# Optimization experiments

Measured on AMD Instinct MI355X. Metric: run time of the kernel, lower is better.

The kernel has to match this reference:

```python
import jax, jax.numpy as jnp
import numpy as np

B, S, D, H, DH = 4, 2048, 1024, 16, 64
INIT_STD = 0.02
IGNORE = -100000.0


def setup_inputs() -> dict:
    key = jax.random.key(0)
    ks = jax.random.split(key, 5)
    x = jax.random.normal(ks[0], (B, S, D), dtype=jnp.float32)
    W_Q = INIT_STD * jax.random.normal(ks[1], (H, D, DH), dtype=jnp.float32)
    W_K = INIT_STD * jax.random.normal(ks[2], (H, D, DH), dtype=jnp.float32)
    W_V = INIT_STD * jax.random.normal(ks[3], (H, D, DH), dtype=jnp.float32)
    W_O = INIT_STD * jax.random.normal(ks[4], (H, DH, D), dtype=jnp.float32)
    b_Q = jnp.zeros((H, DH), dtype=jnp.float32)
    b_K = jnp.zeros((H, DH), dtype=jnp.float32)
    b_V = jnp.zeros((H, DH), dtype=jnp.float32)
    b_O = jnp.zeros((D,), dtype=jnp.float32)
    return {"x": x, "W_Q": W_Q, "b_Q": b_Q, "W_K": W_K, "b_K": b_K,
            "W_V": W_V, "b_V": b_V, "W_O": W_O, "b_O": b_O}


def reference(x, W_Q, b_Q, W_K, b_K, W_V, b_V, W_O, b_O):
    # x: (B, S, D); projections -> (B, S, H, DH)
    Q = jnp.einsum('bqd,hde->bqhe', x, W_Q) + b_Q
    K = jnp.einsum('bkd,hde->bkhe', x, W_K) + b_K
    V = jnp.einsum('bkd,hde->bkhe', x, W_V) + b_V
    d_head = Q.shape[-1]
    # scores: (B, H, Sq, Sk)
    scores = jnp.einsum('bqhe,bkhe->bhqk', Q, K) / np.sqrt(d_head).astype(np.float32)
    s = scores.shape[-1]
    causal = jnp.triu(jnp.ones((s, s), dtype=bool), k=1)
    scores = jnp.where(causal, jnp.float32(IGNORE), scores)
    A = jax.nn.softmax(scores, axis=-1)
    z = jnp.einsum('bhqk,bkhe->bqhe', A, V)
    # output projection: sum over heads + bias
    attn_out = jnp.einsum('bqhe,hed->bqd', z, W_O) + b_O
    return attn_out
```

## Files before the change

kernel.cpp:

```cpp
#include <hip/hip_runtime.h>


#define B_ 4
#define S_ 2048
#define D_ 1024
#define H_ 16
#define DH_ 64

typedef unsigned short ushort_t;
typedef __attribute__((ext_vector_type(4))) short short4v;
typedef __attribute__((ext_vector_type(8))) short short8v;
typedef __attribute__((ext_vector_type(4))) float floatx4;
typedef __attribute__((ext_vector_type(4))) unsigned short ushort4v;

static __device__ __forceinline__ ushort_t f2bf(float f) {
    union { float f; unsigned u; } v; v.f = f;
    unsigned r = v.u + 0x7fffu + ((v.u >> 16) & 1u);
    return (ushort_t)(r >> 16);
}

static __device__ __forceinline__ float fast_exp2(float x) {
#if __has_builtin(__builtin_amdgcn_exp2f)
    return __builtin_amdgcn_exp2f(x);
#else
    return exp2f(x);
#endif
}

static __device__ __forceinline__ unsigned pack_bf16_tr(float lo, float hi) {
    union { float f; unsigned u; } a, b;
    a.f = lo; b.f = hi;
    return __builtin_amdgcn_perm(b.u, a.u, 0x07060302u);
}

static __device__ __forceinline__ void g2lds16(const void* g, void* l) {
    __builtin_amdgcn_global_load_lds(
        (__attribute__((address_space(1))) void*)(unsigned long long)(size_t)g,
        (__attribute__((address_space(3))) void*)(unsigned int)(size_t)l,
        16, 0, 0);
}

__global__ void prep_kernel(const float* __restrict__ x,
                            const float* __restrict__ wq, const float* __restrict__ wk,
                            const float* __restrict__ wv, const float* __restrict__ wo,
                            ushort_t* __restrict__ xb, ushort_t* __restrict__ wt,
                            ushort_t* __restrict__ wot) {
    __shared__ float tile[32][33];
    int bid = blockIdx.x;
    int tid = threadIdx.x;
    if (bid < 8192) {
        int i = (bid * 256 + tid) * 4;
        float4 v = *(const float4*)&x[i];
        ushort4v o;
        o[0] = f2bf(v.x); o[1] = f2bf(v.y); o[2] = f2bf(v.z); o[3] = f2bf(v.w);
        *(ushort4v*)&xb[i] = o;
        return;
    }
    const float* src;
    ushort_t* d;
    int C, r0, c0;
    if (bid < 11264) {
        int t = bid - 8192;
        int z = t / 64, r = t % 64;
        src = (z < 16 ? wq : (z < 32 ? wk : wv)) + (size_t)(z & 15) * 65536;
        d = wt + (size_t)z * 65536;
        C = 64; r0 = (r >> 1) * 32; c0 = (r & 1) * 32;
    } else {
        int t = bid - 11264;
        int z = t / 64, r = t % 64;
        src = wo + (size_t)z * 65536;
        d = wot + (size_t)z * 64;
        C = 1024; r0 = (r & 1) * 32; c0 = (r >> 1) * 32;
    }
    int tx = tid & 31, ty = tid >> 5;
#pragma unroll
    for (int i = 0; i < 4; ++i)
        tile[ty + i * 8][tx] = src[(size_t)(r0 + ty + i * 8) * C + c0 + tx];
    __syncthreads();
#pragma unroll
    for (int i = 0; i < 4; ++i)
        d[(size_t)(c0 + ty + i * 8) * 1024 + r0 + tx] = f2bf(tile[tx][ty + i * 8]);
}


#define GQ_BAR() __builtin_amdgcn_s_barrier()
#define GQ_VM4 do { asm volatile("s_waitcnt vmcnt(4)"); __builtin_amdgcn_sched_barrier(0); } while (0)
#define GQ_VM1 do { asm volatile("s_waitcnt vmcnt(1)"); __builtin_amdgcn_sched_barrier(0); } while (0)
#define GQ_VM0 do { asm volatile("s_waitcnt vmcnt(0)"); __builtin_amdgcn_sched_barrier(0); } while (0)
#define GQ_WAITLG do { asm volatile("s_waitcnt lgkmcnt(0)"); __builtin_amdgcn_sched_barrier(0); } while (0)

#define GQ_READS_B(KB)                                                          \
    _Pragma("unroll") for (int nt = 0; nt < 4; ++nt)                            \
        bfr[KB][nt] = *(const short8v*)&cB[(wn * 64 + nt * 16) * 64 + ((KB) ? kb1 : kb0)];

#define GQ_READS_A(MH, KB)                                                      \
    _Pragma("unroll") for (int i = 0; i < 2; ++i)                               \
        af[i] = *(const short8v*)&cA[(wm * 64 + ((MH) * 2 + i) * 16) * 64 + ((KB) ? kb1 : kb0)];

#define GQ_MFMA(MH, KB)                                                         \
    GQ_WAITLG;                                                                  \
    __builtin_amdgcn_s_setprio(1);                                              \
    _Pragma("unroll") for (int i = 0; i < 2; ++i)                               \
        _Pragma("unroll") for (int nt = 0; nt < 4; ++nt)                        \
            acc[(MH) * 2 + i][nt] = __builtin_amdgcn_mfma_f32_16x16x32_bf16(    \
                af[i], bfr[KB][nt], acc[(MH) * 2 + i][nt], 0, 0, 0);            \
    __builtin_amdgcn_s_setprio(0);                                              \
    __builtin_amdgcn_sched_barrier(0);

#define GQ_KSTEP(CA, CB, S1, S2, S3, S4, WMID, WEND) do {                       \
    const ushort_t* cA = (CA); const ushort_t* cB = (CB);                       \
    short8v af[2]; short8v bfr[2][4];                                           \
    GQ_READS_B(0) GQ_READS_A(0, 0) S1; GQ_BAR();                                \
    GQ_MFMA(0, 0) GQ_BAR();                                                     \
    GQ_READS_B(1) GQ_READS_A(0, 1) S2; GQ_BAR();                                \
    GQ_MFMA(0, 1) WMID; GQ_BAR();                                               \
    GQ_READS_A(1, 0) S3; GQ_BAR();                                              \
    GQ_MFMA(1, 0) GQ_BAR();                                                     \
    GQ_READS_A(1, 1) S4; GQ_BAR();                                              \
    GQ_MFMA(1, 1) WEND; GQ_BAR();                                               \
} while (0)

__global__ __launch_bounds__(512, 2) void gemm_qkv(const ushort_t* __restrict__ A,
                                                   const ushort_t* __restrict__ Wt,
                                                   const float* __restrict__ bq,
                                                   const float* __restrict__ bk,
                                                   const float* __restrict__ bv,
                                                   ushort_t* __restrict__ Qw,
                                                   ushort_t* __restrict__ Kw,
                                                   ushort_t* __restrict__ Vw) {
    __shared__ ushort_t sA[2][128 * 64];
    __shared__ ushort_t sB[2][256 * 64];
    const int tid = threadIdx.x;
    const int lane = tid & 63, w = tid >> 6;
    const int lq = lane & 15, quad = lane >> 4;
    const int wm = w >> 2, wn = w & 3;
    const int m0 = blockIdx.x * 128, n0 = blockIdx.y * 256;

    const int kb0 = lq * 64 + ((quad ^ (lq & 7)) << 3);
    const int kb1 = lq * 64 + (((4 | quad) ^ (lq & 7)) << 3);

    const int uRA = ((w >> 2) << 6) + (w & 3) * 8;

    auto stageA1 = [&](ushort_t* dst, int kk, int R0) __attribute__((always_inline)) {
        int rr = R0 + (lane >> 3);
        int cc = (lane & 7) ^ (rr & 7);
        g2lds16(&A[(size_t)(m0 + rr) * 1024 + kk + cc * 8], &dst[R0 * 64]);
    };
    auto stageB1 = [&](ushort_t* dst, int kk, int R0) __attribute__((always_inline)) {
        int rr = R0 + (lane >> 3);
        int cc = (lane & 7) ^ (rr & 7);
        g2lds16(&Wt[(size_t)(n0 + rr) * 1024 + kk + cc * 8], &dst[R0 * 64]);
    };

    floatx4 acc[4][4] = {};

    stageA1(sA[0], 0, uRA);
    stageB1(sB[0], 0, w * 32);
    stageB1(sB[0], 0, w * 32 + 8);
    stageB1(sB[0], 0, w * 32 + 16);
    stageB1(sB[0], 0, w * 32 + 24);
    stageA1(sA[0], 0, uRA + 32);
    GQ_VM1;
    GQ_BAR();

    int p = 0;
    for (int t = 0; t < 15; ++t) {
        const int kk = (t + 1) * 64;
        ushort_t* nA = sA[p ^ 1];
        ushort_t* nB = sB[p ^ 1];
        GQ_KSTEP(sA[p], sB[p],
                 { stageA1(nA, kk, uRA); stageB1(nB, kk, w * 32); },
                 { stageB1(nB, kk, w * 32 + 8); stageB1(nB, kk, w * 32 + 16); },
                 { stageB1(nB, kk, w * 32 + 24); },
                 { stageA1(nA, kk, uRA + 32); },
                 GQ_VM4, GQ_VM1);
        p ^= 1;
    }
    GQ_KSTEP(sA[1], sB[1], (void)0, (void)0, (void)0, (void)0, GQ_VM0, (void)0);

    const int mat = blockIdx.y >> 2;
    const float* bias = mat == 0 ? bq : (mat == 1 ? bk : bv);
    const int colbase = (blockIdx.y & 3) * 256 + wn * 64;
    float bias_v[4];
#pragma unroll
    for (int nt = 0; nt < 4; ++nt) bias_v[nt] = bias[colbase + nt * 16 + lq];

#pragma unroll
    for (int mt = 0; mt < 4; ++mt) {
#pragma unroll
        for (int nt = 0; nt < 4; ++nt) {
            int row0 = m0 + wm * 64 + mt * 16 + quad * 4;
            int col = colbase + nt * 16 + lq;
            int h = col >> 6, e = col & 63;
            if (mat == 2) {
                int b = row0 >> 11, s = row0 & 2047;
                ushort4v pk;
#pragma unroll
                for (int rg = 0; rg < 4; ++rg) pk[rg] = f2bf(acc[mt][nt][rg] + bias_v[nt]);
                *(ushort4v*)&Vw[((size_t)((b << 4) | h) * 64 + e) * 2048 + s] = pk;
            } else {
                ushort_t* Du = mat == 0 ? Qw : Kw;
#pragma unroll
                for (int rg = 0; rg < 4; ++rg) {
                    int row = row0 + rg;
                    int b = row >> 11, s = row & 2047;
                    float v = acc[mt][nt][rg] + bias_v[nt];
                    if (mat == 0) v *= 0.18033688011112042f;
                    Du[((size_t)((b << 4) | h) * 2048 + s) * 64 + e] = f2bf(v);
                }
            }
        }
    }
}

#define VROW 140
__global__ __launch_bounds__(256) void attn_kernel(const ushort_t* __restrict__ Q,
                                                   const ushort_t* __restrict__ Kg,
                                                   const ushort_t* __restrict__ Vt,
                                                   ushort_t* __restrict__ Z) {
    __shared__ ushort_t sK[2][128 * 64];
    __shared__ ushort_t sV[64 * VROW];
    const int tid = threadIdx.x;
    const int lane = tid & 63, w = tid >> 6;
    const int lq = lane & 15, quad = lane >> 4;
    const int bh = blockIdx.x;
    const int b = bh >> 4, h = bh & 15;
    const ushort_t* Qp = Q + (size_t)bh * S_ * DH_;
    const ushort_t* Kp = Kg + (size_t)bh * S_ * DH_;
    const ushort_t* Vp = Vt + (size_t)bh * DH_ * S_;

    const int kbase0 = lq * 64 + ((quad ^ (lq & 7)) << 3);
    const int kbase1 = lq * 64 + (((4 | quad) ^ (lq & 7)) << 3);
    const int vbase = lq * VROW + quad * 4;
    const int vr = w * 16 + (lane >> 2);
    const int vc = (lane & 3) * 32;

    const floatx4 fzero = {0.f, 0.f, 0.f, 0.f};

    auto stageK = [&](int kt, int bs) __attribute__((always_inline)) {
        ushort_t* dK = sK[bs];
#pragma unroll
        for (int p = 0; p < 4; ++p) {
            int rrk = w * 32 + p * 8 + (lane >> 3);
            int ck = (lane & 7) ^ (rrk & 7);
            g2lds16(&Kp[(size_t)(kt * 128 + rrk) * 64 + ck * 8], &dK[(w * 32 + p * 8) * 64]);
        }
    };
    auto loadV = [&](int kt, short8v* vr4) __attribute__((always_inline)) {
        const ushort_t* src = &Vp[(size_t)vr * 2048 + kt * 128 + vc];
#pragma unroll
        for (int j = 0; j < 4; ++j) vr4[j] = *(const short8v*)&src[j * 8];
    };
    auto writeV = [&](const short8v* vr4) __attribute__((always_inline)) {
        ushort_t* dst = &sV[vr * VROW + vc];
#pragma unroll
        for (int j = 0; j < 4; ++j) *(short8v*)&dst[j * 8] = vr4[j];
    };

    for (int pass = 0; pass < 2; ++pass) {
        const int qt = pass == 0 ? (int)blockIdx.y : 15 - (int)blockIdx.y;
        const int q0 = qt * 128;

        short8v qf[2][2];
#pragma unroll
        for (int qi = 0; qi < 2; ++qi)
#pragma unroll
            for (int ks = 0; ks < 2; ++ks)
                qf[qi][ks] = *(const short8v*)&Qp[(size_t)(q0 + w * 32 + qi * 16 + lq) * DH_ + ks * 32 + quad * 8];

        float l_i[2] = {0.f, 0.f};
        floatx4 o[2][4] = {};
        short8v vreg[4];

        stageK(0, 0);
        loadV(0, vreg);

        for (int kt = 0; kt <= qt; ++kt) {
            const bool diag = (kt == qt);
            const ushort_t* cK = sK[kt & 1];

            __syncthreads();
            writeV(vreg);
            if (kt < qt) {
                stageK(kt + 1, (kt + 1) & 1);
                loadV(kt + 1, vreg);
            }

            floatx4 st[8][2];
            __builtin_amdgcn_s_setprio(1);
#pragma unroll
            for (int si = 0; si < 8; ++si) {
                short8v a0 = *(const short8v*)&cK[kbase0 + si * 1024];
                short8v a1 = *(const short8v*)&cK[kbase1 + si * 1024];
#pragma unroll
                for (int qi = 0; qi < 2; ++qi) {
                    st[si][qi] = __builtin_amdgcn_mfma_f32_16x16x32_bf16(a0, qf[qi][0], fzero, 0, 0, 0);
                    st[si][qi] = __builtin_amdgcn_mfma_f32_16x16x32_bf16(a1, qf[qi][1], st[si][qi], 0, 0, 0);
                }
            }
            __builtin_amdgcn_s_setprio(0);

            short4v pf[8][2];
#pragma unroll
            for (int qi = 0; qi < 2; ++qi) {
                const int qg = q0 + w * 32 + qi * 16 + lq;
                float lsum = 0.f;
#pragma unroll
                for (int si = 0; si < 8; ++si) {
                    float p[4];
#pragma unroll
                    for (int rg = 0; rg < 4; ++rg) {
                        float v = st[si][qi][rg];
                        if (diag) {
                            int sg = kt * 128 + si * 16 + quad * 4 + rg;
                            if (sg > qg) v = -1e30f;
                        }
                        p[rg] = fast_exp2(v);
                        lsum += p[rg];
                    }
                    union { unsigned u[2]; short4v v4; } pk;
                    pk.u[0] = pack_bf16_tr(p[0], p[1]);
                    pk.u[1] = pack_bf16_tr(p[2], p[3]);
                    pf[si][qi] = pk.v4;
                }
                l_i[qi] += lsum;
            }

            __syncthreads();

            __builtin_amdgcn_s_setprio(1);
#pragma unroll
            for (int ksp = 0; ksp < 8; ++ksp) {
#pragma unroll
                for (int et = 0; et < 4; ++et) {
                    short4v vf = *(const short4v*)&sV[vbase + et * (16 * VROW) + ksp * 16];
#pragma unroll
                    for (int qi = 0; qi < 2; ++qi)
                        o[qi][et] = __builtin_amdgcn_mfma_f32_16x16x16bf16_1k(pf[ksp][qi], vf, o[qi][et], 0, 0, 0);
                }
            }
            __builtin_amdgcn_s_setprio(0);
        }

#pragma unroll
        for (int qi = 0; qi < 2; ++qi) {
            float lf = l_i[qi];
            lf += __shfl_xor(lf, 16);
            lf += __shfl_xor(lf, 32);
            float linv[4];
#pragma unroll
            for (int rg = 0; rg < 4; ++rg) linv[rg] = 1.0f / __shfl(lf, quad * 4 + rg);
#pragma unroll
            for (int et = 0; et < 4; ++et) {
#pragma unroll
                for (int rg = 0; rg < 4; ++rg) {
                    int qg = q0 + w * 32 + qi * 16 + quad * 4 + rg;
                    int e = et * 16 + lq;
                    Z[((size_t)(b * S_ + qg) * H_ + h) * DH_ + e] = f2bf(o[qi][et][rg] * linv[rg]);
                }
            }
        }
    }
}

__global__ __launch_bounds__(256) void gemm_o(const ushort_t* __restrict__ A,
                                              const ushort_t* __restrict__ Bt,
                                              const float* __restrict__ bias,
                                              float* __restrict__ Dst) {
    __shared__ ushort_t sA[128 * 64];
    __shared__ ushort_t sB[128 * 64];
    const int tid = threadIdx.x;
    const int lane = tid & 63, w = tid >> 6;
    const int lq = lane & 15, quad = lane >> 4;
    const int wm = w >> 1, wn = w & 1;
    const int m0 = blockIdx.x * 128, n0 = blockIdx.y * 128;

    floatx4 acc[4][4] = {};

    for (int k0 = 0; k0 < 1024; k0 += 64) {
        __syncthreads();
#pragma unroll
        for (int p = 0; p < 4; ++p) {
            int rr = w * 32 + p * 8 + (lane >> 3);
            int cc = (lane & 7) ^ (rr & 7);
            g2lds16(&A[(size_t)(m0 + rr) * 1024 + k0 + cc * 8], &sA[(w * 32 + p * 8) * 64]);
            g2lds16(&Bt[(size_t)(n0 + rr) * 1024 + k0 + cc * 8], &sB[(w * 32 + p * 8) * 64]);
        }
        __syncthreads();
#pragma unroll
        for (int ks = 0; ks < 2; ++ks) {
            short8v af[4], bfr[4];
#pragma unroll
            for (int t = 0; t < 4; ++t) {
                int ma = wm * 64 + t * 16 + lq;
                af[t] = *(const short8v*)&sA[ma * 64 + ((((ks << 2) | quad) ^ (ma & 7)) << 3)];
                int nb = wn * 64 + t * 16 + lq;
                bfr[t] = *(const short8v*)&sB[nb * 64 + ((((ks << 2) | quad) ^ (nb & 7)) << 3)];
            }
#pragma unroll
            for (int mt = 0; mt < 4; ++mt)
#pragma unroll
                for (int nt = 0; nt < 4; ++nt)
                    acc[mt][nt] = __builtin_amdgcn_mfma_f32_16x16x32_bf16(af[mt], bfr[nt], acc[mt][nt], 0, 0, 0);
        }
    }

    float bias_v[4];
#pragma unroll
    for (int nt = 0; nt < 4; ++nt) bias_v[nt] = bias[n0 + wn * 64 + nt * 16 + lq];

#pragma unroll
    for (int mt = 0; mt < 4; ++mt) {
#pragma unroll
        for (int nt = 0; nt < 4; ++nt) {
            int row0 = m0 + wm * 64 + mt * 16 + quad * 4;
            int col = n0 + wn * 64 + nt * 16 + lq;
#pragma unroll
            for (int rg = 0; rg < 4; ++rg)
                Dst[(size_t)(row0 + rg) * 1024 + col] = acc[mt][nt][rg] + bias_v[nt];
        }
    }
}

extern "C" void kernel_launch(void* const* d_in, const int* in_sizes, int n_in,
                              void* d_out, int out_size, void* d_ws, size_t ws_size,
                              hipStream_t stream) {
    const float* x  = (const float*)d_in[0];
    const float* wq = (const float*)d_in[1];
    const float* bq = (const float*)d_in[2];
    const float* wk = (const float*)d_in[3];
    const float* bk = (const float*)d_in[4];
    const float* wv = (const float*)d_in[5];
    const float* bv = (const float*)d_in[6];
    const float* wo = (const float*)d_in[7];
    const float* bo = (const float*)d_in[8];

    char* ws = (char*)d_ws;
    size_t off = 0;
    ushort_t* xb  = (ushort_t*)(ws + off); off += (size_t)8192 * 1024 * 2;
    ushort_t* wt  = (ushort_t*)(ws + off); off += (size_t)3 * 1024 * 1024 * 2;
    ushort_t* wot = (ushort_t*)(ws + off); off += (size_t)1024 * 1024 * 2;
    ushort_t* Qw  = (ushort_t*)(ws + off); off += (size_t)8192 * 1024 * 2;
    ushort_t* Kw  = (ushort_t*)(ws + off); off += (size_t)8192 * 1024 * 2;
    ushort_t* Vw  = (ushort_t*)(ws + off); off += (size_t)8192 * 1024 * 2;
    ushort_t* Zw  = (ushort_t*)(ws + off); off += (size_t)8192 * 1024 * 2;

    prep_kernel<<<12288, 256, 0, stream>>>(x, wq, wk, wv, wo, xb, wt, wot);
    gemm_qkv<<<dim3(64, 12), 512, 0, stream>>>(xb, wt, bq, bk, bv, Qw, Kw, Vw);
    attn_kernel<<<dim3(64, 8), 256, 0, stream>>>(Qw, Kw, Vw, Zw);
    gemm_o<<<dim3(64, 8), 256, 0, stream>>>(Zw, wot, bo, (float*)d_out);
}
```

Baseline: 262.6 us.

## Reuse pipelined QKV GEMM body for output projection; split attention pairs into single tiles

The output-projection GEMM now uses the same double-buffered 128x256 tile with 512 threads and an interleaved MFMA/load schedule as the QKV GEMM, factored into a shared macro. The attention kernel no longer pairs a light and a heavy causal query tile per block. It launches one block per query tile, heaviest first, with a launch-bounds occupancy hint of 3 and no s_setprio calls. This aims to hide load latency in the O GEMM and improve attention occupancy and scheduling, at the cost of some load imbalance and fewer O-GEMM blocks.

```diff
diff --git a/kernel.cpp b/kernel.cpp
--- a/kernel.cpp
+++ b/kernel.cpp
@@ -120,6 +120,30 @@
     GQ_MFMA(1, 1) WEND; GQ_BAR();                                               \
 } while (0)
 
+#define GQ_BODY(APTR, BPTR)                                                     \
+    stageA1(sA[0], 0, uRA);                                                     \
+    stageB1(sB[0], 0, w * 32);                                                  \
+    stageB1(sB[0], 0, w * 32 + 8);                                              \
+    stageB1(sB[0], 0, w * 32 + 16);                                             \
+    stageB1(sB[0], 0, w * 32 + 24);                                             \
+    stageA1(sA[0], 0, uRA + 32);                                                \
+    GQ_VM1;                                                                     \
+    GQ_BAR();                                                                   \
+    int p = 0;                                                                  \
+    for (int t = 0; t < 15; ++t) {                                              \
+        const int kk = (t + 1) * 64;                                            \
+        ushort_t* nA = sA[p ^ 1];                                               \
+        ushort_t* nB = sB[p ^ 1];                                               \
+        GQ_KSTEP(sA[p], sB[p],                                                  \
+                 { stageA1(nA, kk, uRA); stageB1(nB, kk, w * 32); },            \
+                 { stageB1(nB, kk, w * 32 + 8); stageB1(nB, kk, w * 32 + 16); },\
+                 { stageB1(nB, kk, w * 32 + 24); },                             \
+                 { stageA1(nA, kk, uRA + 32); },                                \
+                 GQ_VM4, GQ_VM1);                                               \
+        p ^= 1;                                                                 \
+    }                                                                           \
+    GQ_KSTEP(sA[1], sB[1], (void)0, (void)0, (void)0, (void)0, GQ_VM0, (void)0);
+
 __global__ __launch_bounds__(512, 2) void gemm_qkv(const ushort_t* __restrict__ A,
                                                    const ushort_t* __restrict__ Wt,
                                                    const float* __restrict__ bq,
@@ -154,29 +178,7 @@
 
     floatx4 acc[4][4] = {};
 
-    stageA1(sA[0], 0, uRA);
-    stageB1(sB[0], 0, w * 32);
-    stageB1(sB[0], 0, w * 32 + 8);
-    stageB1(sB[0], 0, w * 32 + 16);
-    stageB1(sB[0], 0, w * 32 + 24);
-    stageA1(sA[0], 0, uRA + 32);
-    GQ_VM1;
-    GQ_BAR();
-
-    int p = 0;
-    for (int t = 0; t < 15; ++t) {
-        const int kk = (t + 1) * 64;
-        ushort_t* nA = sA[p ^ 1];
-        ushort_t* nB = sB[p ^ 1];
-        GQ_KSTEP(sA[p], sB[p],
-                 { stageA1(nA, kk, uRA); stageB1(nB, kk, w * 32); },
-                 { stageB1(nB, kk, w * 32 + 8); stageB1(nB, kk, w * 32 + 16); },
-                 { stageB1(nB, kk, w * 32 + 24); },
-                 { stageA1(nA, kk, uRA + 32); },
-                 GQ_VM4, GQ_VM1);
-        p ^= 1;
-    }
-    GQ_KSTEP(sA[1], sB[1], (void)0, (void)0, (void)0, (void)0, GQ_VM0, (void)0);
+    GQ_BODY(A, Wt)
 
     const int mat = blockIdx.y >> 2;
     const float* bias = mat == 0 ? bq : (mat == 1 ? bk : bv);
@@ -214,10 +216,10 @@
 }
 
 #define VROW 140
-__global__ __launch_bounds__(256) void attn_kernel(const ushort_t* __restrict__ Q,
-                                                   const ushort_t* __restrict__ Kg,
-                                                   const ushort_t* __restrict__ Vt,
-                                                   ushort_t* __restrict__ Z) {
+__global__ __launch_bounds__(256, 3) void attn_kernel(const ushort_t* __restrict__ Q,
+                                                      const ushort_t* __restrict__ Kg,
+                                                      const ushort_t* __restrict__ Vt,
+                                                      ushort_t* __restrict__ Z) {
     __shared__ ushort_t sK[2][128 * 64];
     __shared__ ushort_t sV[64 * VROW];
     const int tid = threadIdx.x;
@@ -257,164 +259,148 @@
         for (int j = 0; j < 4; ++j) *(short8v*)&dst[j * 8] = vr4[j];
     };
 
-    for (int pass = 0; pass < 2; ++pass) {
-        const int qt = pass == 0 ? (int)blockIdx.y : 15 - (int)blockIdx.y;
-        const int q0 = qt * 128;
-
-        short8v qf[2][2];
-#pragma unroll
-        for (int qi = 0; qi < 2; ++qi)
-#pragma unroll
-            for (int ks = 0; ks < 2; ++ks)
-                qf[qi][ks] = *(const short8v*)&Qp[(size_t)(q0 + w * 32 + qi * 16 + lq) * DH_ + ks * 32 + quad * 8];
-
-        float l_i[2] = {0.f, 0.f};
-        floatx4 o[2][4] = {};
-        short8v vreg[4];
-
-        stageK(0, 0);
-        loadV(0, vreg);
-
-        for (int kt = 0; kt <= qt; ++kt) {
-            const bool diag = (kt == qt);
-            const ushort_t* cK = sK[kt & 1];
-
-            __syncthreads();
-            writeV(vreg);
-            if (kt < qt) {
-                stageK(kt + 1, (kt + 1) & 1);
-                loadV(kt + 1, vreg);
+    const int qt = 15 - (int)blockIdx.y;
+    const int q0 = qt * 128;
+
+    short8v qf[2][2];
+#pragma unroll
+    for (int qi = 0; qi < 2; ++qi)
+#pragma unroll
+        for (int ks = 0; ks < 2; ++ks)
+            qf[qi][ks] = *(const short8v*)&Qp[(size_t)(q0 + w * 32 + qi * 16 + lq) * DH_ + ks * 32 + quad * 8];
+
+    float l_i[2] = {0.f, 0.f};
+    floatx4 o[2][4] = {};
+    short8v vreg[4];
+
+    stageK(0, 0);
+    loadV(0, vreg);
+
+    for (int kt = 0; kt <= qt; ++kt) {
+        const bool diag = (kt == qt);
+        const ushort_t* cK = sK[kt & 1];
+
+        __syncthreads();
+        writeV(vreg);
+        if (kt < qt) {
+            stageK(kt + 1, (kt + 1) & 1);
+            loadV(kt + 1, vreg);
+        }
+
+        floatx4 st[8][2];
+#pragma unroll
+        for (int si = 0; si < 8; ++si) {
+            short8v a0 = *(const short8v*)&cK[kbase0 + si * 1024];
+            short8v a1 = *(const short8v*)&cK[kbase1 + si * 1024];
+#pragma unroll
+            for (int qi = 0; qi < 2; ++qi) {
+                st[si][qi] = __builtin_amdgcn_mfma_f32_16x16x32_bf16(a0, qf[qi][0], fzero, 0, 0, 0);
+                st[si][qi] = __builtin_amdgcn_mfma_f32_16x16x32_bf16(a1, qf[qi][1], st[si][qi], 0, 0, 0);
             }
-
-            floatx4 st[8][2];
-            __builtin_amdgcn_s_setprio(1);
+        }
+
+        short4v pf[8][2];
+#pragma unroll
+        for (int qi = 0; qi < 2; ++qi) {
+            const int qg = q0 + w * 32 + qi * 16 + lq;
+            float lsum = 0.f;
 #pragma unroll
             for (int si = 0; si < 8; ++si) {
-                short8v a0 = *(const short8v*)&cK[kbase0 + si * 1024];
-                short8v a1 = *(const short8v*)&cK[kbase1 + si * 1024];
-#pragma unroll
-                for (int qi = 0; qi < 2; ++qi) {
-                    st[si][qi] = __builtin_amdgcn_mfma_f32_16x16x32_bf16(a0, qf[qi][0], fzero, 0, 0, 0);
-                    st[si][qi] = __builtin_amdgcn_mfma_f32_16x16x32_bf16(a1, qf[qi][1], st[si][qi], 0, 0, 0);
+                float p[4];
+#pragma unroll
+                for (int rg = 0; rg < 4; ++rg) {
+                    float v = st[si][qi][rg];
+                    if (diag) {
+                        int sg = kt * 128 + si * 16 + quad * 4 + rg;
+                        if (sg > qg) v = -1e30f;
+                    }
+                    p[rg] = fast_exp2(v);
+                    lsum += p[rg];
                 }
+                union { unsigned u[2]; short4v v4; } pk;
+                pk.u[0] = pack_bf16_tr(p[0], p[1]);
+                pk.u[1] = pack_bf16_tr(p[2], p[3]);
+                pf[si][qi] = pk.v4;
             }
-            __builtin_amdgcn_s_setprio(0);
-
-            short4v pf[8][2];
-#pragma unroll
-            for (int qi = 0; qi < 2; ++qi) {
-                const int qg = q0 + w * 32 + qi * 16 + lq;
-                float lsum = 0.f;
-#pragma unroll
-                for (int si = 0; si < 8; ++si) {
-                    float p[4];
-#pragma unroll
-                    for (int rg = 0; rg < 4; ++rg) {
-                        float v = st[si][qi][rg];
-                        if (diag) {
-                            int sg = kt * 128 + si * 16 + quad * 4 + rg;
-                            if (sg > qg) v = -1e30f;
-                        }
-                        p[rg] = fast_exp2(v);
-                        lsum += p[rg];
-                    }
-                    union { unsigned u[2]; short4v v4; } pk;
-                    pk.u[0] = pack_bf16_tr(p[0], p[1]);
-                    pk.u[1] = pack_bf16_tr(p[2], p[3]);
-                    pf[si][qi] = pk.v4;
-                }
-                l_i[qi] += lsum;
+            l_i[qi] += lsum;
+        }
+
+        __syncthreads();
+
+#pragma unroll
+        for (int ksp = 0; ksp < 8; ++ksp) {
+#pragma unroll
+            for (int et = 0; et < 4; ++et) {
+                short4v vf = *(const short4v*)&sV[vbase + et * (16 * VROW) + ksp * 16];
+#pragma unroll
+                for (int qi = 0; qi < 2; ++qi)
+                    o[qi][et] = __builtin_amdgcn_mfma_f32_16x16x16bf16_1k(pf[ksp][qi], vf, o[qi][et], 0, 0, 0);
             }
-
-            __syncthreads();
-
-            __builtin_amdgcn_s_setprio(1);
-#pragma unroll
-            for (int ksp = 0; ksp < 8; ++ksp) {
-#pragma unroll
-                for (int et = 0; et < 4; ++et) {
-                    short4v vf = *(const short4v*)&sV[vbase + et * (16 * VROW) + ksp * 16];
-#pragma unroll
-                    for (int qi = 0; qi < 2; ++qi)
-                        o[qi][et] = __builtin_amdgcn_mfma_f32_16x16x16bf16_1k(pf[ksp][qi], vf, o[qi][et], 0, 0, 0);
-                }
+        }
+    }
+
+#pragma unroll
+    for (int qi = 0; qi < 2; ++qi) {
+        float lf = l_i[qi];
+        lf += __shfl_xor(lf, 16);
+        lf += __shfl_xor(lf, 32);
+        float linv[4];
+#pragma unroll
+        for (int rg = 0; rg < 4; ++rg) linv[rg] = 1.0f / __shfl(lf, quad * 4 + rg);
+#pragma unroll
+        for (int et = 0; et < 4; ++et) {
+#pragma unroll
+            for (int rg = 0; rg < 4; ++rg) {
+                int qg = q0 + w * 32 + qi * 16 + quad * 4 + rg;
+                int e = et * 16 + lq;
+                Z[((size_t)(b * S_ + qg) * H_ + h) * DH_ + e] = f2bf(o[qi][et][rg] * linv[rg]);
             }
-            __builtin_amdgcn_s_setprio(0);
-        }
-
-#pragma unroll
-        for (int qi = 0; qi < 2; ++qi) {
-            float lf = l_i[qi];
-            lf += __shfl_xor(lf, 16);
-            lf += __shfl_xor(lf, 32);
-            float linv[4];
-#pragma unroll
-            for (int rg = 0; rg < 4; ++rg) linv[rg] = 1.0f / __shfl(lf, quad * 4 + rg);
-#pragma unroll
-            for (int et = 0; et < 4; ++et) {
-#pragma unroll
-                for (int rg = 0; rg < 4; ++rg) {
-                    int qg = q0 + w * 32 + qi * 16 + quad * 4 + rg;
-                    int e = et * 16 + lq;
-                    Z[((size_t)(b * S_ + qg) * H_ + h) * DH_ + e] = f2bf(o[qi][et][rg] * linv[rg]);
-                }
-            }
-        }
-    }
-}
-
-__global__ __launch_bounds__(256) void gemm_o(const ushort_t* __restrict__ A,
-                                              const ushort_t* __restrict__ Bt,
-                                              const float* __restrict__ bias,
-                                              float* __restrict__ Dst) {
-    __shared__ ushort_t sA[128 * 64];
-    __shared__ ushort_t sB[128 * 64];
+        }
+    }
+}
+
+__global__ __launch_bounds__(512, 2) void gemm_o(const ushort_t* __restrict__ A,
+                                                 const ushort_t* __restrict__ Bt,
+                                                 const float* __restrict__ bias,
+                                                 float* __restrict__ Dst) {
+    __shared__ ushort_t sA[2][128 * 64];
+    __shared__ ushort_t sB[2][256 * 64];
     const int tid = threadIdx.x;
     const int lane = tid & 63, w = tid >> 6;
     const int lq = lane & 15, quad = lane >> 4;
-    const int wm = w >> 1, wn = w & 1;
-    const int m0 = blockIdx.x * 128, n0 = blockIdx.y * 128;
+    const int wm = w >> 2, wn = w & 3;
+    const int m0 = blockIdx.x * 128, n0 = blockIdx.y * 256;
+
+    const int kb0 = lq * 64 + ((quad ^ (lq & 7)) << 3);
+    const int kb1 = lq * 64 + (((4 | quad) ^ (lq & 7)) << 3);
+    const int uRA = ((w >> 2) << 6) + (w & 3) * 8;
+
+    auto stageA1 = [&](ushort_t* dst, int kk, int R0) __attribute__((always_inline)) {
+        int rr = R0 + (lane >> 3);
+        int cc = (lane & 7) ^ (rr & 7);
+        g2lds16(&A[(size_t)(m0 + rr) * 1024 + kk + cc * 8], &dst[R0 * 64]);
+    };
+    auto stageB1 = [&](ushort_t* dst, int kk, int R0) __attribute__((always_inline)) {
+        int rr = R0 + (lane >> 3);
+        int cc = (lane & 7) ^ (rr & 7);
+        g2lds16(&Bt[(size_t)(n0 + rr) * 1024 + kk + cc * 8], &dst[R0 * 64]);
+    };
 
     floatx4 acc[4][4] = {};
 
-    for (int k0 = 0; k0 < 1024; k0 += 64) {
-        __syncthreads();
-#pragma unroll
-        for (int p = 0; p < 4; ++p) {
-            int rr = w * 32 + p * 8 + (lane >> 3);
-            int cc = (lane & 7) ^ (rr & 7);
-            g2lds16(&A[(size_t)(m0 + rr) * 1024 + k0 + cc * 8], &sA[(w * 32 + p * 8) * 64]);
-            g2lds16(&Bt[(size_t)(n0 + rr) * 1024 + k0 + cc * 8], &sB[(w * 32 + p * 8) * 64]);
-        }
-        __syncthreads();
-#pragma unroll
-        for (int ks = 0; ks < 2; ++ks) {
-            short8v af[4], bfr[4];
-#pragma unroll
-            for (int t = 0; t < 4; ++t) {
-                int ma = wm * 64 + t * 16 + lq;
-                af[t] = *(const short8v*)&sA[ma * 64 + ((((ks << 2) | quad) ^ (ma & 7)) << 3)];
-                int nb = wn * 64 + t * 16 + lq;
-                bfr[t] = *(const short8v*)&sB[nb * 64 + ((((ks << 2) | quad) ^ (nb & 7)) << 3)];
-            }
-#pragma unroll
-            for (int mt = 0; mt < 4; ++mt)
-#pragma unroll
-                for (int nt = 0; nt < 4; ++nt)
-                    acc[mt][nt] = __builtin_amdgcn_mfma_f32_16x16x32_bf16(af[mt], bfr[nt], acc[mt][nt], 0, 0, 0);
-        }
-    }
-
+    GQ_BODY(A, Bt)
+
+    const int colbase = n0 + wn * 64;
     float bias_v[4];
 #pragma unroll
-    for (int nt = 0; nt < 4; ++nt) bias_v[nt] = bias[n0 + wn * 64 + nt * 16 + lq];
+    for (int nt = 0; nt < 4; ++nt) bias_v[nt] = bias[colbase + nt * 16 + lq];
 
 #pragma unroll
     for (int mt = 0; mt < 4; ++mt) {
 #pragma unroll
         for (int nt = 0; nt < 4; ++nt) {
             int row0 = m0 + wm * 64 + mt * 16 + quad * 4;
-            int col = n0 + wn * 64 + nt * 16 + lq;
+            int col = colbase + nt * 16 + lq;
 #pragma unroll
             for (int rg = 0; rg < 4; ++rg)
                 Dst[(size_t)(row0 + rg) * 1024 + col] = acc[mt][nt][rg] + bias_v[nt];
@@ -447,6 +433,6 @@
 
     prep_kernel<<<12288, 256, 0, stream>>>(x, wq, wk, wv, wo, xb, wt, wot);
     gemm_qkv<<<dim3(64, 12), 512, 0, stream>>>(xb, wt, bq, bk, bv, Qw, Kw, Vw);
-    attn_kernel<<<dim3(64, 8), 256, 0, stream>>>(Qw, Kw, Vw, Zw);
-    gemm_o<<<dim3(64, 8), 256, 0, stream>>>(Zw, wot, bo, (float*)d_out);
-}
+    attn_kernel<<<dim3(64, 16), 256, 0, stream>>>(Qw, Kw, Vw, Zw);
+    gemm_o<<<dim3(64, 4), 512, 0, stream>>>(Zw, wot, bo, (float*)d_out);
+}
```

After: 295.8 us. 1.13x slower.

## Shrink QKV GEMM tile to 128x128 with 4 waves and drop attention setprio

Applied to the files above, without the earlier changes.

The QKV projection GEMM moves from 512-thread blocks with 128x256 tiles to 256-thread blocks with 128x128 tiles. The grid doubles in the N dimension, and the staging loads and vmcnt waits are rebalanced to match. This gives more, smaller blocks and less LDS per block, which should improve occupancy and wave scheduling, at the cost of reloading the A tile more often. Separately, the s_setprio raises around the MFMA sections in the attention kernel are removed.

```diff
diff --git a/kernel.cpp b/kernel.cpp
--- a/kernel.cpp
+++ b/kernel.cpp
@@ -85,7 +85,7 @@
 
 #define GQ_BAR() __builtin_amdgcn_s_barrier()
 #define GQ_VM4 do { asm volatile("s_waitcnt vmcnt(4)"); __builtin_amdgcn_sched_barrier(0); } while (0)
-#define GQ_VM1 do { asm volatile("s_waitcnt vmcnt(1)"); __builtin_amdgcn_sched_barrier(0); } while (0)
+#define GQ_VM2 do { asm volatile("s_waitcnt vmcnt(2)"); __builtin_amdgcn_sched_barrier(0); } while (0)
 #define GQ_VM0 do { asm volatile("s_waitcnt vmcnt(0)"); __builtin_amdgcn_sched_barrier(0); } while (0)
 #define GQ_WAITLG do { asm volatile("s_waitcnt lgkmcnt(0)"); __builtin_amdgcn_sched_barrier(0); } while (0)
 
@@ -120,7 +120,7 @@
     GQ_MFMA(1, 1) WEND; GQ_BAR();                                               \
 } while (0)
 
-__global__ __launch_bounds__(512, 2) void gemm_qkv(const ushort_t* __restrict__ A,
+__global__ __launch_bounds__(256, 2) void gemm_qkv(const ushort_t* __restrict__ A,
                                                    const ushort_t* __restrict__ Wt,
                                                    const float* __restrict__ bq,
                                                    const float* __restrict__ bk,
@@ -129,24 +129,25 @@
                                                    ushort_t* __restrict__ Kw,
                                                    ushort_t* __restrict__ Vw) {
     __shared__ ushort_t sA[2][128 * 64];
-    __shared__ ushort_t sB[2][256 * 64];
+    __shared__ ushort_t sB[2][128 * 64];
     const int tid = threadIdx.x;
     const int lane = tid & 63, w = tid >> 6;
     const int lq = lane & 15, quad = lane >> 4;
-    const int wm = w >> 2, wn = w & 3;
-    const int m0 = blockIdx.x * 128, n0 = blockIdx.y * 256;
+    const int wm = w >> 1, wn = w & 1;
+    const int m0 = blockIdx.x * 128, n0 = blockIdx.y * 128;
 
     const int kb0 = lq * 64 + ((quad ^ (lq & 7)) << 3);
     const int kb1 = lq * 64 + (((4 | quad) ^ (lq & 7)) << 3);
 
-    const int uRA = ((w >> 2) << 6) + (w & 3) * 8;
-
-    auto stageA1 = [&](ushort_t* dst, int kk, int R0) __attribute__((always_inline)) {
+    const int uA = ((w >> 1) << 6) + ((w & 1) << 4);
+    const int bR = w * 32;
+
+    auto stA = [&](ushort_t* dst, int kk, int R0) __attribute__((always_inline)) {
         int rr = R0 + (lane >> 3);
         int cc = (lane & 7) ^ (rr & 7);
         g2lds16(&A[(size_t)(m0 + rr) * 1024 + kk + cc * 8], &dst[R0 * 64]);
     };
-    auto stageB1 = [&](ushort_t* dst, int kk, int R0) __attribute__((always_inline)) {
+    auto stB = [&](ushort_t* dst, int kk, int R0) __attribute__((always_inline)) {
         int rr = R0 + (lane >> 3);
         int cc = (lane & 7) ^ (rr & 7);
         g2lds16(&Wt[(size_t)(n0 + rr) * 1024 + kk + cc * 8], &dst[R0 * 64]);
@@ -154,13 +155,11 @@
 
     floatx4 acc[4][4] = {};
 
-    stageA1(sA[0], 0, uRA);
-    stageB1(sB[0], 0, w * 32);
-    stageB1(sB[0], 0, w * 32 + 8);
-    stageB1(sB[0], 0, w * 32 + 16);
-    stageB1(sB[0], 0, w * 32 + 24);
-    stageA1(sA[0], 0, uRA + 32);
-    GQ_VM1;
+    stA(sA[0], 0, uA); stA(sA[0], 0, uA + 8);
+    stB(sB[0], 0, bR); stB(sB[0], 0, bR + 8);
+    stB(sB[0], 0, bR + 16); stB(sB[0], 0, bR + 24);
+    stA(sA[0], 0, uA + 32); stA(sA[0], 0, uA + 40);
+    GQ_VM2;
     GQ_BAR();
 
     int p = 0;
@@ -169,18 +168,18 @@
         ushort_t* nA = sA[p ^ 1];
         ushort_t* nB = sB[p ^ 1];
         GQ_KSTEP(sA[p], sB[p],
-                 { stageA1(nA, kk, uRA); stageB1(nB, kk, w * 32); },
-                 { stageB1(nB, kk, w * 32 + 8); stageB1(nB, kk, w * 32 + 16); },
-                 { stageB1(nB, kk, w * 32 + 24); },
-                 { stageA1(nA, kk, uRA + 32); },
-                 GQ_VM4, GQ_VM1);
+                 { stA(nA, kk, uA); stA(nA, kk, uA + 8); },
+                 { stB(nB, kk, bR); stB(nB, kk, bR + 8); },
+                 { stB(nB, kk, bR + 16); stB(nB, kk, bR + 24); },
+                 { stA(nA, kk, uA + 32); stA(nA, kk, uA + 40); },
+                 GQ_VM4, GQ_VM2);
         p ^= 1;
     }
     GQ_KSTEP(sA[1], sB[1], (void)0, (void)0, (void)0, (void)0, GQ_VM0, (void)0);
 
-    const int mat = blockIdx.y >> 2;
+    const int mat = blockIdx.y >> 3;
     const float* bias = mat == 0 ? bq : (mat == 1 ? bk : bv);
-    const int colbase = (blockIdx.y & 3) * 256 + wn * 64;
+    const int colbase = (blockIdx.y & 7) * 128 + wn * 64;
     float bias_v[4];
 #pragma unroll
     for (int nt = 0; nt < 4; ++nt) bias_v[nt] = bias[colbase + nt * 16 + lq];
@@ -287,7 +286,6 @@
             }
 
             floatx4 st[8][2];
-            __builtin_amdgcn_s_setprio(1);
 #pragma unroll
             for (int si = 0; si < 8; ++si) {
                 short8v a0 = *(const short8v*)&cK[kbase0 + si * 1024];
@@ -298,7 +296,6 @@
                     st[si][qi] = __builtin_amdgcn_mfma_f32_16x16x32_bf16(a1, qf[qi][1], st[si][qi], 0, 0, 0);
                 }
             }
-            __builtin_amdgcn_s_setprio(0);
 
             short4v pf[8][2];
 #pragma unroll
@@ -328,7 +325,6 @@
 
             __syncthreads();
 
-            __builtin_amdgcn_s_setprio(1);
 #pragma unroll
             for (int ksp = 0; ksp < 8; ++ksp) {
 #pragma unroll
@@ -339,7 +335,6 @@
                         o[qi][et] = __builtin_amdgcn_mfma_f32_16x16x16bf16_1k(pf[ksp][qi], vf, o[qi][et], 0, 0, 0);
                 }
             }
-            __builtin_amdgcn_s_setprio(0);
         }
 
 #pragma unroll
@@ -446,7 +441,7 @@
     ushort_t* Zw  = (ushort_t*)(ws + off); off += (size_t)8192 * 1024 * 2;
 
     prep_kernel<<<12288, 256, 0, stream>>>(x, wq, wk, wv, wo, xb, wt, wot);
-    gemm_qkv<<<dim3(64, 12), 512, 0, stream>>>(xb, wt, bq, bk, bv, Qw, Kw, Vw);
+    gemm_qkv<<<dim3(64, 24), 256, 0, stream>>>(xb, wt, bq, bk, bv, Qw, Kw, Vw);
     attn_kernel<<<dim3(64, 8), 256, 0, stream>>>(Qw, Kw, Vw, Zw);
     gemm_o<<<dim3(64, 8), 256, 0, stream>>>(Zw, wot, bo, (float*)d_out);
 }
```

Result: faster. 253.4 us (-3.5%).
